# Kernel optimization log

Hardware: AMD Instinct MI355X
Metric: run time of the kernel (lower is better)

The kernel has to match this reference:

```python
import jax, jax.numpy as jnp
import numpy as np

N_OBJ = 4096      # n_objects (fixed node count; fc1 consumes flattened node features)
F_IN = 256        # in_feats
H = 256           # n_hidden
C = 128           # n_classes
NE = 8            # number of edge types
EPT = 131072      # edges per etype (avg in-degree 32)


def setup_inputs() -> dict:
    key = jax.random.key(0)
    ks = jax.random.split(key, 16)
    s = 0.02  # weight init scale
    inp = {
        "feat": jax.random.normal(ks[0], (N_OBJ, F_IN), dtype=jnp.float32),
        "edges": jax.random.randint(ks[1], (NE, 2, EPT), 0, N_OBJ, dtype=jnp.int64),
        # 3 hetero layers: layer0 (F_IN->H), layers 1,2 (H->H), each with per-etype Linear
        "W0": jax.random.normal(ks[2], (NE, H, F_IN), dtype=jnp.float32) * s,
        "b0": jnp.zeros((NE, H), dtype=jnp.float32),
        "W1": jax.random.normal(ks[3], (NE, H, H), dtype=jnp.float32) * s,
        "b1": jnp.zeros((NE, H), dtype=jnp.float32),
        "W2": jax.random.normal(ks[4], (NE, H, H), dtype=jnp.float32) * s,
        "b2": jnp.zeros((NE, H), dtype=jnp.float32),
        "fc1_w": jax.random.normal(ks[5], (H, N_OBJ * H), dtype=jnp.float32) * 0.002,
        "fc1_b": jnp.zeros((H,), dtype=jnp.float32),
        "fc2_w": jax.random.normal(ks[6], (C, H), dtype=jnp.float32) * s,
        "fc2_b": jnp.zeros((C,), dtype=jnp.float32),
    }
    return inp


def _hetero_layer(h, W, b, edges):
    # Per-etype linear: Wh[e] = h @ W[e].T + b[e]   -> [NE, N, H]
    Wh = jnp.einsum('nf,ehf->enh', h, W) + b[:, None, :]

    def per_etype(wh, src, dst):
        msg = wh[src]                                            # gather: [EPT, H]
        ssum = jax.ops.segment_sum(msg, dst, num_segments=N_OBJ)  # [N, H]
        deg = jax.ops.segment_sum(jnp.ones_like(dst, dtype=wh.dtype), dst,
                                  num_segments=N_OBJ)             # [N]
        return ssum / jnp.maximum(deg, 1.0)[:, None]              # mean reduce

    agg = jax.vmap(per_etype)(Wh, edges[:, 0], edges[:, 1])  # [NE, N, H]
    # multi_update_all cross-type aggregator 'sum', then activation (relu)
    return jax.nn.relu(agg.sum(axis=0))


def reference(feat, edges, W0, b0, W1, b1, W2, b2, fc1_w, fc1_b, fc2_w, fc2_b):
    h = _hetero_layer(feat, W0, b0, edges)
    h = _hetero_layer(h, W1, b1, edges)
    h = _hetero_layer(h, W2, b2, edges)
    flat = h.reshape(-1)                          # [N*H]
    z = jax.nn.relu(fc1_w @ flat + fc1_b)         # [H]
    out = jax.nn.sigmoid(fc2_w @ z + fc2_b)       # [C]
    return out
```

## Files before the change

### kernel.cpp

```cpp
#include <hip/hip_runtime.h>
#include <math.h>

#define N_OBJ 4096
#define F     256
#define NE    8
#define EPT   131072
#define KCAT  (NE * F)
#define C_OUT 128
#define FC1_K (N_OBJ * F)

typedef __attribute__((ext_vector_type(8))) short s8v;
typedef __attribute__((ext_vector_type(4))) float f4v;

__device__ inline float bf2f(unsigned short u) {
    unsigned int x = ((unsigned int)u) << 16;
    return __builtin_bit_cast(float, x);
}
__device__ inline unsigned short f2bf(float f) {
    unsigned int x = __builtin_bit_cast(unsigned int, f);
    x += 0x7fff + ((x >> 16) & 1);
    return (unsigned short)(x >> 16);
}


__global__ __launch_bounds__(256) void k_count_deg(const int* __restrict__ edges,
                                                   int* __restrict__ deg) {
    int gid = blockIdx.x * 256 + threadIdx.x;
    int e = gid >> 17;
    int i = gid & (EPT - 1);
    int dst = edges[(e * 2 + 1) * EPT + i];
    atomicAdd(&deg[e * N_OBJ + dst], 1);
}

__global__ __launch_bounds__(256) void k_scan(const int* __restrict__ deg,
                                              int* __restrict__ rowptr,
                                              int* __restrict__ cursor,
                                              float* __restrict__ invdeg) {
    int e = blockIdx.x;
    int t = threadIdx.x;
    __shared__ int part[256];
    int local[16];
    int base = e * N_OBJ + t * 16;
    int s = 0;
#pragma unroll
    for (int i = 0; i < 16; ++i) { local[i] = deg[base + i]; s += local[i]; }
    part[t] = s;
    __syncthreads();
    for (int off = 1; off < 256; off <<= 1) {
        int v = (t >= off) ? part[t - off] : 0;
        __syncthreads();
        part[t] += v;
        __syncthreads();
    }
    int run = part[t] - s;
#pragma unroll
    for (int i = 0; i < 16; ++i) {
        rowptr[base + i] = run;
        cursor[base + i] = run;
        invdeg[base + i] = 1.0f / fmaxf((float)local[i], 1.0f);
        run += local[i];
    }
}

__global__ __launch_bounds__(256) void k_fill(const int* __restrict__ edges,
                                              int* __restrict__ cursor,
                                              int* __restrict__ col) {
    int gid = blockIdx.x * 256 + threadIdx.x;
    int e = gid >> 17;
    int i = gid & (EPT - 1);
    int src = edges[(e * 2 + 0) * EPT + i];
    int dst = edges[(e * 2 + 1) * EPT + i];
    int pos = atomicAdd(&cursor[e * N_OBJ + dst], 1);
    col[e * EPT + pos] = src;
}

__global__ __launch_bounds__(256) void k_bmask(const int* __restrict__ deg,
                                               unsigned int* __restrict__ bmask) {
    int n = blockIdx.x * 256 + threadIdx.x;
    unsigned int m = 0;
#pragma unroll
    for (int e = 0; e < NE; ++e) m |= (deg[e * N_OBJ + n] > 0) ? (1u << e) : 0u;
    bmask[n] = m;
}

#define WQ4 (NE * F * F / 4)
#define FQ4 (N_OBJ * F / 4)
__global__ __launch_bounds__(256) void k_cvt_all(const float* __restrict__ W0,
                                                 const float* __restrict__ W1,
                                                 const float* __restrict__ W2,
                                                 const float* __restrict__ feat,
                                                 unsigned short* __restrict__ Wb0,
                                                 unsigned short* __restrict__ Wb1,
                                                 unsigned short* __restrict__ Wb2,
                                                 unsigned short* __restrict__ featb) {
    int i = blockIdx.x * 256 + threadIdx.x;
    const float* s;
    unsigned short* d;
    int j;
    if (i < WQ4)            { s = W0;   d = Wb0;   j = i; }
    else if (i < 2 * WQ4)   { s = W1;   d = Wb1;   j = i - WQ4; }
    else if (i < 3 * WQ4)   { s = W2;   d = Wb2;   j = i - 2 * WQ4; }
    else                    { s = feat; d = featb; j = i - 3 * WQ4; }
    float4 v = ((const float4*)s)[j];
    ushort4 o;
    o.x = f2bf(v.x); o.y = f2bf(v.y); o.z = f2bf(v.z); o.w = f2bf(v.w);
    ((ushort4*)d)[j] = o;
}

__global__ __launch_bounds__(256) void k_aggregate(const unsigned short* __restrict__ h_in,
                                                   const int* __restrict__ rowptr,
                                                   const int* __restrict__ deg,
                                                   const int* __restrict__ col,
                                                   const float* __restrict__ invdeg,
                                                   unsigned short* __restrict__ ah) {
    int wid = blockIdx.x * 4 + (threadIdx.x >> 6);
    int lane = threadIdx.x & 63;
    int e = wid >> 12;
    int n = wid & (N_OBJ - 1);
    int beg = rowptr[wid];
    int cnt = deg[wid];
    const int* cl = col + e * EPT + beg;
    const ushort4* h4 = (const ushort4*)h_in;
    float a0 = 0.f, a1 = 0.f, a2 = 0.f, a3 = 0.f;
    int k = 0;
    for (; k + 8 <= cnt; k += 8) {
        int s0 = cl[k],     s1 = cl[k + 1], s2 = cl[k + 2], s3 = cl[k + 3];
        int s4 = cl[k + 4], s5 = cl[k + 5], s6 = cl[k + 6], s7 = cl[k + 7];
        ushort4 v0 = h4[s0 * 64 + lane];
        ushort4 v1 = h4[s1 * 64 + lane];
        ushort4 v2 = h4[s2 * 64 + lane];
        ushort4 v3 = h4[s3 * 64 + lane];
        ushort4 v4 = h4[s4 * 64 + lane];
        ushort4 v5 = h4[s5 * 64 + lane];
        ushort4 v6 = h4[s6 * 64 + lane];
        ushort4 v7 = h4[s7 * 64 + lane];
        a0 += bf2f(v0.x) + bf2f(v1.x) + bf2f(v2.x) + bf2f(v3.x)
            + bf2f(v4.x) + bf2f(v5.x) + bf2f(v6.x) + bf2f(v7.x);
        a1 += bf2f(v0.y) + bf2f(v1.y) + bf2f(v2.y) + bf2f(v3.y)
            + bf2f(v4.y) + bf2f(v5.y) + bf2f(v6.y) + bf2f(v7.y);
        a2 += bf2f(v0.z) + bf2f(v1.z) + bf2f(v2.z) + bf2f(v3.z)
            + bf2f(v4.z) + bf2f(v5.z) + bf2f(v6.z) + bf2f(v7.z);
        a3 += bf2f(v0.w) + bf2f(v1.w) + bf2f(v2.w) + bf2f(v3.w)
            + bf2f(v4.w) + bf2f(v5.w) + bf2f(v6.w) + bf2f(v7.w);
    }
    for (; k < cnt; ++k) {
        ushort4 v = h4[cl[k] * 64 + lane];
        a0 += bf2f(v.x); a1 += bf2f(v.y); a2 += bf2f(v.z); a3 += bf2f(v.w);
    }
    float sc = invdeg[wid];
    ushort4 o;
    o.x = f2bf(a0 * sc); o.y = f2bf(a1 * sc); o.z = f2bf(a2 * sc); o.w = f2bf(a3 * sc);
    ((ushort4*)ah)[n * (KCAT / 4) + e * (F / 4) + lane] = o;
}

template <int OUTBF>
__global__ __launch_bounds__(128) void k_gemm(const unsigned short* __restrict__ A,
                                              const unsigned short* __restrict__ Wb,
                                              const float* __restrict__ bias,
                                              const unsigned int* __restrict__ bmask,
                                              void* __restrict__ Cout) {
    __shared__ short As[32][40];
    __shared__ short Bs[64][40];
    int m0 = blockIdx.x * 32, n0 = blockIdx.y * 64;
    int t = threadIdx.x;
    int wave = t >> 6, lane = t & 63;
    int r = lane & 15, g = lane >> 4;
    int arow = t >> 2, aseg = t & 3;
    int brow = t >> 1, bseg = (t & 1) * 2;
    f4v acc[2][2];
#pragma unroll
    for (int i = 0; i < 2; ++i)
#pragma unroll
        for (int j = 0; j < 2; ++j) acc[i][j] = (f4v){0.f, 0.f, 0.f, 0.f};
    const short* Ap = (const short*)A;
    const short* Wp = (const short*)Wb;
    for (int k0 = 0; k0 < KCAT; k0 += 32) {
        int e = k0 >> 8, f0 = k0 & 255;
        s8v va = *(const s8v*)(Ap + (size_t)(m0 + arow) * KCAT + k0 + aseg * 8);
        const short* wbase = Wp + (size_t)e * F * F + (size_t)(n0 + brow) * F + f0;
        s8v vb0 = *(const s8v*)(wbase + bseg * 8);
        s8v vb1 = *(const s8v*)(wbase + bseg * 8 + 8);
        __syncthreads();
        *(s8v*)&As[arow][aseg * 8] = va;
        *(s8v*)&Bs[brow][bseg * 8] = vb0;
        *(s8v*)&Bs[brow][bseg * 8 + 8] = vb1;
        __syncthreads();
        s8v bf0 = *(const s8v*)&Bs[wave * 32 + r][g * 8];
        s8v bf1 = *(const s8v*)&Bs[wave * 32 + 16 + r][g * 8];
#pragma unroll
        for (int m = 0; m < 2; ++m) {
            s8v af = *(const s8v*)&As[m * 16 + r][g * 8];
            acc[m][0] = __builtin_amdgcn_mfma_f32_16x16x32_bf16(af, bf0, acc[m][0], 0, 0, 0);
            acc[m][1] = __builtin_amdgcn_mfma_f32_16x16x32_bf16(af, bf1, acc[m][1], 0, 0, 0);
        }
    }
#pragma unroll
    for (int nn = 0; nn < 2; ++nn) {
        int coln = n0 + wave * 32 + nn * 16 + r;
        float bcol[NE];
#pragma unroll
        for (int e = 0; e < NE; ++e) bcol[e] = bias[e * F + coln];
#pragma unroll
        for (int m = 0; m < 2; ++m) {
#pragma unroll
            for (int reg = 0; reg < 4; ++reg) {
                int mm = m0 + m * 16 + g * 4 + reg;
                unsigned int msk = bmask[mm];
                float v = acc[m][nn][reg];
#pragma unroll
                for (int e = 0; e < NE; ++e)
                    if ((msk >> e) & 1) v += bcol[e];
                v = fmaxf(v, 0.f);
                if (OUTBF) ((unsigned short*)Cout)[(size_t)mm * F + coln] = f2bf(v);
                else       ((float*)Cout)[(size_t)mm * F + coln] = v;
            }
        }
    }
}

__global__ __launch_bounds__(256) void k_fc1(const float* __restrict__ Wf,
                                             const float* __restrict__ flat,
                                             float* __restrict__ zpart) {
    int c = blockIdx.x;
    int j = blockIdx.y;
    int t = threadIdx.x;
    const float4* wp = (const float4*)(Wf + (size_t)j * FC1_K + (size_t)c * 65536);
    const float4* fp = (const float4*)(flat + (size_t)c * 65536);
    float s = 0.0f;
#pragma unroll 8
    for (int it = 0; it < 64; ++it) {
        int q = it * 256 + t;
        float4 w4 = wp[q];
        float4 x4 = fp[q];
        s = fmaf(w4.x, x4.x, s);
        s = fmaf(w4.y, x4.y, s);
        s = fmaf(w4.z, x4.z, s);
        s = fmaf(w4.w, x4.w, s);
    }
#pragma unroll
    for (int off = 32; off > 0; off >>= 1) s += __shfl_down(s, off, 64);
    __shared__ float red[4];
    if ((t & 63) == 0) red[t >> 6] = s;
    __syncthreads();
    if (t == 0) zpart[c * 256 + j] = red[0] + red[1] + red[2] + red[3];
}

__global__ __launch_bounds__(256) void k_final(const float* __restrict__ zpart,
                                               const float* __restrict__ fc1_b,
                                               const float* __restrict__ fc2_w,
                                               const float* __restrict__ fc2_b,
                                               float* __restrict__ out) {
    __shared__ float z[256];
    int t = threadIdx.x;
    float s = fc1_b[t];
#pragma unroll
    for (int c = 0; c < 16; ++c) s += zpart[c * 256 + t];
    z[t] = fmaxf(s, 0.0f);
    __syncthreads();
    if (t < C_OUT) {
        float acc = fc2_b[t];
        for (int k = 0; k < 256; ++k) acc = fmaf(fc2_w[t * 256 + k], z[k], acc);
        out[t] = 1.0f / (1.0f + expf(-acc));
    }
}

extern "C" void kernel_launch(void* const* d_in, const int* in_sizes, int n_in,
                              void* d_out, int out_size, void* d_ws, size_t ws_size,
                              hipStream_t stream) {
    const float* feat  = (const float*)d_in[0];
    const int*   edges = (const int*)d_in[1];
    const float* W0    = (const float*)d_in[2];
    const float* b0    = (const float*)d_in[3];
    const float* W1    = (const float*)d_in[4];
    const float* b1    = (const float*)d_in[5];
    const float* W2    = (const float*)d_in[6];
    const float* b2    = (const float*)d_in[7];
    const float* fc1_w = (const float*)d_in[8];
    const float* fc1_b = (const float*)d_in[9];
    const float* fc2_w = (const float*)d_in[10];
    const float* fc2_b = (const float*)d_in[11];
    float* out = (float*)d_out;

    char* ws = (char*)d_ws;
    size_t off = 0;
    auto alloc = [&](size_t bytes) {
        void* p = ws + off;
        off = (off + bytes + 255) & ~(size_t)255;
        return p;
    };
    int*            deg    = (int*)            alloc(NE * N_OBJ * 4);
    int*            rowptr = (int*)            alloc(NE * N_OBJ * 4);
    int*            cursor = (int*)            alloc(NE * N_OBJ * 4);
    float*          invdeg = (float*)          alloc(NE * N_OBJ * 4);
    int*            col    = (int*)            alloc(NE * EPT * 4);
    unsigned int*   bmask  = (unsigned int*)   alloc(N_OBJ * 4);
    float*          zpart  = (float*)          alloc(16 * 256 * 4);
    unsigned short* Wb0    = (unsigned short*) alloc((size_t)NE * F * F * 2);
    unsigned short* Wb1    = (unsigned short*) alloc((size_t)NE * F * F * 2);
    unsigned short* Wb2    = (unsigned short*) alloc((size_t)NE * F * F * 2);
    unsigned short* featb  = (unsigned short*) alloc((size_t)N_OBJ * F * 2);
    unsigned short* h_ba   = (unsigned short*) alloc((size_t)N_OBJ * F * 2);
    unsigned short* h_bb   = (unsigned short*) alloc((size_t)N_OBJ * F * 2);
    float*          h_f32  = (float*)          alloc((size_t)N_OBJ * F * 4);
    unsigned short* ah     = (unsigned short*) alloc((size_t)N_OBJ * KCAT * 2);
    (void)ws_size; (void)in_sizes; (void)n_in; (void)out_size;

    hipMemsetAsync(deg, 0, NE * N_OBJ * 4, stream);
    k_count_deg<<<NE * EPT / 256, 256, 0, stream>>>(edges, deg);
    k_scan<<<NE, 256, 0, stream>>>(deg, rowptr, cursor, invdeg);
    k_fill<<<NE * EPT / 256, 256, 0, stream>>>(edges, cursor, col);
    k_bmask<<<N_OBJ / 256, 256, 0, stream>>>(deg, bmask);
    k_cvt_all<<<(3 * WQ4 + FQ4) / 256, 256, 0, stream>>>(W0, W1, W2, feat,
                                                         Wb0, Wb1, Wb2, featb);

    dim3 ggrid(N_OBJ / 32, F / 64);
    int agrid = NE * N_OBJ / 4;

    k_aggregate<<<agrid, 256, 0, stream>>>(featb, rowptr, deg, col, invdeg, ah);
    k_gemm<1><<<ggrid, 128, 0, stream>>>(ah, Wb0, b0, bmask, h_ba);
    k_aggregate<<<agrid, 256, 0, stream>>>(h_ba, rowptr, deg, col, invdeg, ah);
    k_gemm<1><<<ggrid, 128, 0, stream>>>(ah, Wb1, b1, bmask, h_bb);
    k_aggregate<<<agrid, 256, 0, stream>>>(h_bb, rowptr, deg, col, invdeg, ah);
    k_gemm<0><<<ggrid, 128, 0, stream>>>(ah, Wb2, b2, bmask, h_f32);

    dim3 fgrid(16, 256);
    k_fc1<<<fgrid, 256, 0, stream>>>(fc1_w, h_f32, zpart);
    k_final<<<1, 256, 0, stream>>>(zpart, fc1_b, fc2_w, fc2_b, out);
}
```

Baseline: 522.2 us.

## Double-buffer swizzled 64x64 GEMM tiles and stage fc1 activations in shared memory

The aggregated-feature GEMM now uses 64x64 output tiles with 256 threads, a K-step of 64, double-buffered LDS with an XOR swizzle, and prefetches the next tile while MFMAs run. This halves the barriers per K and raises reuse of each loaded A/B fragment. fc1 now loads a 16K-element chunk of the flattened activations into LDS once and computes 8 output rows per block, so activation re-reads drop. The cost is more partial sums (64 chunks) for the final reduction and higher LDS use per block, which may limit occupancy.

Result: faster. 484.8 us (-7.2%).

```diff
diff --git a/kernel.cpp b/kernel.cpp
--- a/kernel.cpp
+++ b/kernel.cpp
@@ -8,6 +8,9 @@
 #define KCAT  (NE * F)
 #define C_OUT 128
 #define FC1_K (N_OBJ * F)
+#define FCH   16384
+#define FNCH  (FC1_K / FCH)
+#define FRJ   8
 
 typedef __attribute__((ext_vector_type(8))) short s8v;
 typedef __attribute__((ext_vector_type(4))) float f4v;
@@ -20,6 +23,9 @@
     unsigned int x = __builtin_bit_cast(unsigned int, f);
     x += 0x7fff + ((x >> 16) & 1);
     return (unsigned short)(x >> 16);
+}
+__device__ __forceinline__ int swz(int row, int k8) {
+    return (row * 64 + k8 * 8) ^ ((row & 7) << 3);
 }
 
 
@@ -154,66 +160,89 @@
 }
 
 template <int OUTBF>
-__global__ __launch_bounds__(128) void k_gemm(const unsigned short* __restrict__ A,
-                                              const unsigned short* __restrict__ Wb,
-                                              const float* __restrict__ bias,
-                                              const unsigned int* __restrict__ bmask,
-                                              void* __restrict__ Cout) {
-    __shared__ short As[32][40];
-    __shared__ short Bs[64][40];
-    int m0 = blockIdx.x * 32, n0 = blockIdx.y * 64;
+__global__ __launch_bounds__(256, 4) void k_gemm(const unsigned short* __restrict__ A,
+                                                 const unsigned short* __restrict__ Wb,
+                                                 const float* __restrict__ bias,
+                                                 const unsigned int* __restrict__ bmask,
+                                                 void* __restrict__ Cout) {
+    __shared__ short As[2][64 * 64];
+    __shared__ short Bs[2][64 * 64];
+    int m0 = blockIdx.x * 64, n0 = blockIdx.y * 64;
     int t = threadIdx.x;
     int wave = t >> 6, lane = t & 63;
     int r = lane & 15, g = lane >> 4;
-    int arow = t >> 2, aseg = t & 3;
-    int brow = t >> 1, bseg = (t & 1) * 2;
-    f4v acc[2][2];
-#pragma unroll
-    for (int i = 0; i < 2; ++i)
-#pragma unroll
-        for (int j = 0; j < 2; ++j) acc[i][j] = (f4v){0.f, 0.f, 0.f, 0.f};
+    int row0 = t >> 3, seg0 = t & 7;
+    int row1 = row0 + 32;
+    int wA0 = swz(row0, seg0), wA1 = swz(row1, seg0);
+
     const short* Ap = (const short*)A;
     const short* Wp = (const short*)Wb;
-    for (int k0 = 0; k0 < KCAT; k0 += 32) {
-        int e = k0 >> 8, f0 = k0 & 255;
-        s8v va = *(const s8v*)(Ap + (size_t)(m0 + arow) * KCAT + k0 + aseg * 8);
-        const short* wbase = Wp + (size_t)e * F * F + (size_t)(n0 + brow) * F + f0;
-        s8v vb0 = *(const s8v*)(wbase + bseg * 8);
-        s8v vb1 = *(const s8v*)(wbase + bseg * 8 + 8);
+    const short* arp0 = Ap + (size_t)(m0 + row0) * KCAT + seg0 * 8;
+    const short* arp1 = Ap + (size_t)(m0 + row1) * KCAT + seg0 * 8;
+    int brow0 = (n0 + row0) * F + seg0 * 8;
+    int brow1 = (n0 + row1) * F + seg0 * 8;
+
+    f4v acc[4];
+#pragma unroll
+    for (int i = 0; i < 4; ++i) acc[i] = (f4v){0.f, 0.f, 0.f, 0.f};
+
+    {
+        s8v a0 = *(const s8v*)(arp0);
+        s8v a1 = *(const s8v*)(arp1);
+        s8v b0 = *(const s8v*)(Wp + brow0);
+        s8v b1 = *(const s8v*)(Wp + brow1);
+        *(s8v*)&As[0][wA0] = a0; *(s8v*)&As[0][wA1] = a1;
+        *(s8v*)&Bs[0][wA0] = b0; *(s8v*)&Bs[0][wA1] = b1;
+    }
+    __syncthreads();
+#pragma unroll 1
+    for (int ks = 0; ks < 32; ++ks) {
+        int cur = ks & 1;
+        s8v a0, a1, b0, b1;
+        if (ks < 31) {
+            int kb = (ks + 1) * 64;
+            int woff = ((kb >> 8) << 16) + (kb & 255);
+            a0 = *(const s8v*)(arp0 + kb);
+            a1 = *(const s8v*)(arp1 + kb);
+            b0 = *(const s8v*)(Wp + woff + brow0);
+            b1 = *(const s8v*)(Wp + woff + brow1);
+        }
+        const short* as = As[cur];
+        const short* bs = Bs[cur];
+#pragma unroll
+        for (int kk = 0; kk < 2; ++kk) {
+            s8v af = *(const s8v*)&as[swz(wave * 16 + r, kk * 4 + g)];
+#pragma unroll
+            for (int n = 0; n < 4; ++n) {
+                s8v bf = *(const s8v*)&bs[swz(n * 16 + r, kk * 4 + g)];
+                acc[n] = __builtin_amdgcn_mfma_f32_16x16x32_bf16(af, bf, acc[n], 0, 0, 0);
+            }
+        }
+        if (ks < 31) {
+            *(s8v*)&As[cur ^ 1][wA0] = a0; *(s8v*)&As[cur ^ 1][wA1] = a1;
+            *(s8v*)&Bs[cur ^ 1][wA0] = b0; *(s8v*)&Bs[cur ^ 1][wA1] = b1;
+        }
         __syncthreads();
-        *(s8v*)&As[arow][aseg * 8] = va;
-        *(s8v*)&Bs[brow][bseg * 8] = vb0;
-        *(s8v*)&Bs[brow][bseg * 8 + 8] = vb1;
-        __syncthreads();
-        s8v bf0 = *(const s8v*)&Bs[wave * 32 + r][g * 8];
-        s8v bf1 = *(const s8v*)&Bs[wave * 32 + 16 + r][g * 8];
-#pragma unroll
-        for (int m = 0; m < 2; ++m) {
-            s8v af = *(const s8v*)&As[m * 16 + r][g * 8];
-            acc[m][0] = __builtin_amdgcn_mfma_f32_16x16x32_bf16(af, bf0, acc[m][0], 0, 0, 0);
-            acc[m][1] = __builtin_amdgcn_mfma_f32_16x16x32_bf16(af, bf1, acc[m][1], 0, 0, 0);
-        }
-    }
-#pragma unroll
-    for (int nn = 0; nn < 2; ++nn) {
-        int coln = n0 + wave * 32 + nn * 16 + r;
+    }
+    int mb = m0 + wave * 16 + g * 4;
+    unsigned int msk[4];
+#pragma unroll
+    for (int reg = 0; reg < 4; ++reg) msk[reg] = bmask[mb + reg];
+#pragma unroll
+    for (int n = 0; n < 4; ++n) {
+        int coln = n0 + n * 16 + r;
         float bcol[NE];
 #pragma unroll
         for (int e = 0; e < NE; ++e) bcol[e] = bias[e * F + coln];
 #pragma unroll
-        for (int m = 0; m < 2; ++m) {
-#pragma unroll
-            for (int reg = 0; reg < 4; ++reg) {
-                int mm = m0 + m * 16 + g * 4 + reg;
-                unsigned int msk = bmask[mm];
-                float v = acc[m][nn][reg];
-#pragma unroll
-                for (int e = 0; e < NE; ++e)
-                    if ((msk >> e) & 1) v += bcol[e];
-                v = fmaxf(v, 0.f);
-                if (OUTBF) ((unsigned short*)Cout)[(size_t)mm * F + coln] = f2bf(v);
-                else       ((float*)Cout)[(size_t)mm * F + coln] = v;
-            }
+        for (int reg = 0; reg < 4; ++reg) {
+            float v = acc[n][reg];
+#pragma unroll
+            for (int e = 0; e < NE; ++e)
+                if ((msk[reg] >> e) & 1) v += bcol[e];
+            v = fmaxf(v, 0.f);
+            if (OUTBF) ((unsigned short*)Cout)[(size_t)(mb + reg) * F + coln] = f2bf(v);
+            else       ((float*)Cout)[(size_t)(mb + reg) * F + coln] = v;
         }
     }
 }
@@ -221,28 +250,47 @@
 __global__ __launch_bounds__(256) void k_fc1(const float* __restrict__ Wf,
                                              const float* __restrict__ flat,
                                              float* __restrict__ zpart) {
+    __shared__ float xs[FCH];
     int c = blockIdx.x;
-    int j = blockIdx.y;
+    int jg = blockIdx.y;
     int t = threadIdx.x;
-    const float4* wp = (const float4*)(Wf + (size_t)j * FC1_K + (size_t)c * 65536);
-    const float4* fp = (const float4*)(flat + (size_t)c * 65536);
-    float s = 0.0f;
-#pragma unroll 8
-    for (int it = 0; it < 64; ++it) {
-        int q = it * 256 + t;
-        float4 w4 = wp[q];
-        float4 x4 = fp[q];
-        s = fmaf(w4.x, x4.x, s);
-        s = fmaf(w4.y, x4.y, s);
-        s = fmaf(w4.z, x4.z, s);
-        s = fmaf(w4.w, x4.w, s);
-    }
-#pragma unroll
-    for (int off = 32; off > 0; off >>= 1) s += __shfl_down(s, off, 64);
-    __shared__ float red[4];
-    if ((t & 63) == 0) red[t >> 6] = s;
-    __syncthreads();
-    if (t == 0) zpart[c * 256 + j] = red[0] + red[1] + red[2] + red[3];
+    const float4* fp = (const float4*)(flat + (size_t)c * FCH);
+    float4* xs4 = (float4*)xs;
+#pragma unroll
+    for (int q = 0; q < FCH / 4 / 256; ++q) xs4[q * 256 + t] = fp[q * 256 + t];
+    __syncthreads();
+    float accs[FRJ];
+#pragma unroll
+    for (int rr = 0; rr < FRJ; ++rr) {
+        const float4* wp = (const float4*)(Wf + (size_t)(jg * FRJ + rr) * FC1_K
+                                              + (size_t)c * FCH);
+        float s = 0.0f;
+#pragma unroll 4
+        for (int it = 0; it < FCH / 4 / 256; ++it) {
+            int q = it * 256 + t;
+            float4 w4 = wp[q];
+            float4 x4 = xs4[q];
+            s = fmaf(w4.x, x4.x,
+                fmaf(w4.y, x4.y,
+                fmaf(w4.z, x4.z,
+                fmaf(w4.w, x4.w, s))));
+        }
+        accs[rr] = s;
+    }
+    __shared__ float red[4][FRJ];
+    int lane = t & 63, wv = t >> 6;
+#pragma unroll
+    for (int rr = 0; rr < FRJ; ++rr) {
+        float s = accs[rr];
+#pragma unroll
+        for (int off = 32; off > 0; off >>= 1) s += __shfl_down(s, off, 64);
+        if (lane == 0) red[wv][rr] = s;
+    }
+    __syncthreads();
+    if (t < FRJ) {
+        float s = red[0][t] + red[1][t] + red[2][t] + red[3][t];
+        zpart[c * 256 + jg * FRJ + t] = s;
+    }
 }
 
 __global__ __launch_bounds__(256) void k_final(const float* __restrict__ zpart,
@@ -254,7 +302,7 @@
     int t = threadIdx.x;
     float s = fc1_b[t];
 #pragma unroll
-    for (int c = 0; c < 16; ++c) s += zpart[c * 256 + t];
+    for (int c = 0; c < FNCH; ++c) s += zpart[c * 256 + t];
     z[t] = fmaxf(s, 0.0f);
     __syncthreads();
     if (t < C_OUT) {
@@ -294,7 +342,7 @@
     float*          invdeg = (float*)          alloc(NE * N_OBJ * 4);
     int*            col    = (int*)            alloc(NE * EPT * 4);
     unsigned int*   bmask  = (unsigned int*)   alloc(N_OBJ * 4);
-    float*          zpart  = (float*)          alloc(16 * 256 * 4);
+    float*          zpart  = (float*)          alloc(FNCH * 256 * 4);
     unsigned short* Wb0    = (unsigned short*) alloc((size_t)NE * F * F * 2);
     unsigned short* Wb1    = (unsigned short*) alloc((size_t)NE * F * F * 2);
     unsigned short* Wb2    = (unsigned short*) alloc((size_t)NE * F * F * 2);
@@ -313,17 +361,17 @@
     k_cvt_all<<<(3 * WQ4 + FQ4) / 256, 256, 0, stream>>>(W0, W1, W2, feat,
                                                          Wb0, Wb1, Wb2, featb);
 
-    dim3 ggrid(N_OBJ / 32, F / 64);
+    dim3 ggrid(N_OBJ / 64, F / 64);
     int agrid = NE * N_OBJ / 4;
 
     k_aggregate<<<agrid, 256, 0, stream>>>(featb, rowptr, deg, col, invdeg, ah);
-    k_gemm<1><<<ggrid, 128, 0, stream>>>(ah, Wb0, b0, bmask, h_ba);
+    k_gemm<1><<<ggrid, 256, 0, stream>>>(ah, Wb0, b0, bmask, h_ba);
     k_aggregate<<<agrid, 256, 0, stream>>>(h_ba, rowptr, deg, col, invdeg, ah);
-    k_gemm<1><<<ggrid, 128, 0, stream>>>(ah, Wb1, b1, bmask, h_bb);
+    k_gemm<1><<<ggrid, 256, 0, stream>>>(ah, Wb1, b1, bmask, h_bb);
     k_aggregate<<<agrid, 256, 0, stream>>>(h_bb, rowptr, deg, col, invdeg, ah);
-    k_gemm<0><<<ggrid, 128, 0, stream>>>(ah, Wb2, b2, bmask, h_f32);
-
-    dim3 fgrid(16, 256);
+    k_gemm<0><<<ggrid, 256, 0, stream>>>(ah, Wb2, b2, bmask, h_f32);
+
+    dim3 fgrid(FNCH, 256 / FRJ);
     k_fc1<<<fgrid, 256, 0, stream>>>(fc1_w, h_f32, zpart);
     k_final<<<1, 256, 0, stream>>>(zpart, fc1_b, fc2_w, fc2_b, out);
 }
```
